# Optimization experiments

Measured on AMD Instinct MI355X. Metric: run time of the kernel, lower is better.

## Reference

```python
import jax, jax.numpy as jnp
import numpy as np

B, LM, LX, D = 16, 1024, 1024, 768


def setup_inputs() -> dict:
    key = jax.random.key(0)
    k1, k2, k3, k4 = jax.random.split(key, 4)
    main = jax.random.normal(k1, (B, LM, D), dtype=jnp.float32)
    x = jax.random.normal(k2, (B, LX, D), dtype=jnp.float32)
    # keras 'uniform' init ~ U(-0.05, 0.05); scale to keep activations sane
    W = jax.random.uniform(k3, (D, D), dtype=jnp.float32, minval=-0.05, maxval=0.05)
    w = jax.random.uniform(k4, (2 * D, 1), dtype=jnp.float32, minval=-0.05, maxval=0.05)
    return {"main": main, "x": x, "W": W, "w": w}


def reference(main, x, W, w):
    # bilinear co-attention scores: (main @ W) . x^T -> (B, LM, LX)
    proj = jnp.einsum('bmd,de->bme', main, W)            # (B, LM, D)
    scores = jnp.einsum('bme,bne->bmn', proj, x)         # (B, LM, LX) -- no softmax in original
    A = jnp.einsum('bmn,bnd->bmd', scores, x)            # attended features (B, LM, D)
    s = main - A
    m = main * A
    outputs = jnp.concatenate([s, m], axis=-1)           # (B, LM, 2D)
    beta = jnp.einsum('bmk,k->bm', outputs, w[:, 0])     # (B, LM) -- raw, no softmax
    pooled = jnp.einsum('bm,bmk->bk', beta, outputs)     # weighted-sum pooling (B, 2D)
    return pooled
```

## Files before the change

### kernel.cpp

```cpp
#include <hip/hip_runtime.h>

constexpr int kB  = 16;
constexpr int kLM = 1024;
constexpr int kLX = 1024;
constexpr int kD  = 768;

using short8 = __attribute__((ext_vector_type(8))) short;
using f32x4  = __attribute__((ext_vector_type(4))) float;

__device__ __forceinline__ unsigned short f2bf(float f) {
    unsigned u = __float_as_uint(f);
    u = (u + 0x7FFF + ((u >> 16) & 1)) >> 16;
    return (unsigned short)u;
}
__device__ __forceinline__ float bf2f(unsigned short h) {
    return __uint_as_float(((unsigned)h) << 16);
}

__device__ __forceinline__ void gl_lds16(const unsigned short* g, unsigned short* l) {
    auto gp = (const __attribute__((address_space(1))) unsigned int*)g;
    auto lp = (__attribute__((address_space(3))) unsigned int*)l;
    __builtin_amdgcn_global_load_lds(gp, lp, 16, 0, 0);
}

__device__ __forceinline__ void writeChunk(unsigned short* dst, float4 lo, float4 hi) {
    union { short8 v; unsigned short u[8]; } o;
    o.u[0] = f2bf(lo.x); o.u[1] = f2bf(lo.y); o.u[2] = f2bf(lo.z); o.u[3] = f2bf(lo.w);
    o.u[4] = f2bf(hi.x); o.u[5] = f2bf(hi.y); o.u[6] = f2bf(hi.z); o.u[7] = f2bf(hi.w);
    *(short8*)dst = o.v;
}

__device__ __forceinline__ size_t chunk_off(int c, int K) {
    int sr = c >> 3, s = c & 7;
    int tt = s ^ (sr & 7);
    int r  = sr * 2 + (tt >> 2);
    int q  = tt & 3;
    return (size_t)r * K + q * 8;
}

__global__ __launch_bounds__(256) void transpose_cvt_kernel(
    const float* __restrict__ x, unsigned short* __restrict__ xT) {
    __shared__ float tile[64][65];
    const int b  = blockIdx.z;
    const int l0 = blockIdx.x * 64;
    const int d0 = blockIdx.y * 64;
    const int t  = threadIdx.x;
    const int tx = t & 15, ty = t >> 4;
    const float* xb = x + ((size_t)b * kLX + l0) * kD + d0;
#pragma unroll
    for (int p = 0; p < 4; ++p) {
        int r = p * 16 + ty;
        float4 v = *(const float4*)(xb + (size_t)r * kD + tx * 4);
        *(float4*)&tile[r][tx * 4] = v;
    }
    __syncthreads();
    unsigned short* xTb = xT + ((size_t)b * kD + d0) * kLX + l0;
#pragma unroll
    for (int p = 0; p < 4; ++p) {
        int dr = p * 16 + ty;
        ushort4 o;
        o.x = f2bf(tile[tx * 4 + 0][dr]);
        o.y = f2bf(tile[tx * 4 + 1][dr]);
        o.z = f2bf(tile[tx * 4 + 2][dr]);
        o.w = f2bf(tile[tx * 4 + 3][dr]);
        *(ushort4*)(xTb + (size_t)dr * kLX + tx * 4) = o;
    }
}

__global__ __launch_bounds__(256) void cvt2_kernel(
    const float* __restrict__ a, unsigned short* __restrict__ oa, int na8,
    const float* __restrict__ b, unsigned short* __restrict__ ob, int nb8) {
    int i = blockIdx.x * 256 + threadIdx.x;
    const float* src;
    unsigned short* dst;
    if (i < na8) {
        src = a + (size_t)i * 8; dst = oa + (size_t)i * 8;
    } else {
        int j = i - na8;
        if (j >= nb8) return;
        src = b + (size_t)j * 8; dst = ob + (size_t)j * 8;
    }
    float4 lo = *(const float4*)src;
    float4 hi = *(const float4*)(src + 4);
    writeChunk(dst, lo, hi);
}

template <bool SYMM>
__global__ __launch_bounds__(256) void gemm_nt_kernel(
    const unsigned short* __restrict__ A, const unsigned short* __restrict__ B,
    unsigned short* __restrict__ C, int M, int N, int K,
    long sA, long sB, long sC, int gx, int gy) {
    __shared__ unsigned short Asm[3][128 * 32];
    __shared__ unsigned short Bsm[3][128 * 32];

    const int wgid = blockIdx.x;
    const int xcd  = wgid & 7;
    const int kk   = wgid >> 3;
    const int tpb  = gx * gy;
    const int grp  = kk / tpb;
    const int til  = kk - grp * tpb;
    const int b    = grp * 8 + xcd;
    const int bi   = til % gx;
    const int bj   = til / gx;
    if (SYMM && bi < bj) return;
    const int i0 = bi * 128, j0 = bj * 128;

    const int t    = threadIdx.x;
    const int wave = t >> 6, lane = t & 63;
    const int wr = (wave >> 1) * 64, wc = (wave & 1) * 64;
    const int quad = lane >> 4, l15 = lane & 15;

    const unsigned short* Ab = A + (size_t)b * sA + (size_t)i0 * K;
    const unsigned short* Bb = B + (size_t)b * sB + (size_t)j0 * K;

    const int c0 = t, c1 = t + 256;
    const size_t off0 = chunk_off(c0, K);
    const size_t off1 = chunk_off(c1, K);

    const int sfr  = ((l15 & 1) * 4 + quad) ^ ((l15 >> 1) & 7);
    const int aOff = wr * 32 + (l15 >> 1) * 64 + sfr * 8;
    const int bOff = wc * 32 + (l15 >> 1) * 64 + sfr * 8;

    f32x4 acc[4][4];
    const f32x4 z = {0.f, 0.f, 0.f, 0.f};
#pragma unroll
    for (int i = 0; i < 4; ++i)
#pragma unroll
        for (int j = 0; j < 4; ++j) acc[i][j] = z;

    const int T = K >> 5;

    gl_lds16(Ab + off0, Asm[0] + c0 * 8);
    gl_lds16(Ab + off1, Asm[0] + c1 * 8);
    gl_lds16(Bb + off0, Bsm[0] + c0 * 8);
    gl_lds16(Bb + off1, Bsm[0] + c1 * 8);
    if (T > 1) {
        gl_lds16(Ab + off0 + 32, Asm[1] + c0 * 8);
        gl_lds16(Ab + off1 + 32, Asm[1] + c1 * 8);
        gl_lds16(Bb + off0 + 32, Bsm[1] + c0 * 8);
        gl_lds16(Bb + off1 + 32, Bsm[1] + c1 * 8);
    }

    int cur = 0;
    for (int kt = 0; kt < T; ++kt) {
        if (kt + 2 < T) {
            int nb = cur + 2; if (nb >= 3) nb -= 3;
            const size_t k = (size_t)(kt + 2) << 5;
            gl_lds16(Ab + off0 + k, Asm[nb] + c0 * 8);
            gl_lds16(Ab + off1 + k, Asm[nb] + c1 * 8);
            gl_lds16(Bb + off0 + k, Bsm[nb] + c0 * 8);
            gl_lds16(Bb + off1 + k, Bsm[nb] + c1 * 8);
            asm volatile("s_waitcnt vmcnt(8)" ::: "memory");
        } else if (kt + 1 < T) {
            asm volatile("s_waitcnt vmcnt(4)" ::: "memory");
        } else {
            asm volatile("s_waitcnt vmcnt(0)" ::: "memory");
        }
        __builtin_amdgcn_s_barrier();
        asm volatile("" ::: "memory");

        const unsigned short* aP = Asm[cur] + aOff;
        const unsigned short* bP = Bsm[cur] + bOff;
        short8 af[4], bg[4];
#pragma unroll
        for (int i = 0; i < 4; ++i) af[i] = *(const short8*)(aP + i * 512);
#pragma unroll
        for (int j = 0; j < 4; ++j) bg[j] = *(const short8*)(bP + j * 512);
        __builtin_amdgcn_s_setprio(1);
#pragma unroll
        for (int i = 0; i < 4; ++i)
#pragma unroll
            for (int j = 0; j < 4; ++j)
                acc[i][j] = __builtin_amdgcn_mfma_f32_16x16x32_bf16(
                    af[i], bg[j], acc[i][j], 0, 0, 0);
        __builtin_amdgcn_s_setprio(0);
        asm volatile("" ::: "memory");
        __builtin_amdgcn_s_barrier();
        cur = cur + 1; if (cur == 3) cur = 0;
    }

    unsigned short* Cb = C + (size_t)b * sC + (size_t)(i0 + wr) * N + j0 + wc;
#pragma unroll
    for (int i = 0; i < 4; ++i)
#pragma unroll
        for (int j = 0; j < 4; ++j)
#pragma unroll
            for (int r = 0; r < 4; ++r)
                Cb[(size_t)(i * 16 + quad * 4 + r) * N + j * 16 + l15] =
                    f2bf(acc[i][j][r]);

    if (SYMM && bi > bj) {
        unsigned short* Cm = C + (size_t)b * sC + (size_t)(j0 + wc) * N + i0 + wr;
#pragma unroll
        for (int i = 0; i < 4; ++i)
#pragma unroll
            for (int j = 0; j < 4; ++j) {
                ushort4 o;
                o.x = f2bf(acc[i][j][0]);
                o.y = f2bf(acc[i][j][1]);
                o.z = f2bf(acc[i][j][2]);
                o.w = f2bf(acc[i][j][3]);
                *(ushort4*)(Cm + (size_t)(j * 16 + l15) * N + i * 16 + quad * 4) = o;
            }
    }
}

__global__ __launch_bounds__(256) void pool_kernel(
    const float* __restrict__ mainp, const unsigned short* __restrict__ Aout,
    const float* __restrict__ w, float* __restrict__ out) {
    __shared__ float red[4][24][64];
    const int b     = blockIdx.y;
    const int chunk = blockIdx.x;
    const int t     = threadIdx.x;
    const int wave  = t >> 6, lane = t & 63;
    float w1[12], w2[12], ps[12], pm[12];
#pragma unroll
    for (int s = 0; s < 12; ++s) {
        w1[s] = w[s * 64 + lane];
        w2[s] = w[kD + s * 64 + lane];
        ps[s] = 0.f; pm[s] = 0.f;
    }
#pragma unroll
    for (int rr = 0; rr < 4; ++rr) {
        const int row = chunk * 16 + rr * 4 + wave;
        const float* mr = mainp + ((size_t)b * kLM + row) * kD;
        const unsigned short* ar = Aout + ((size_t)b * kLM + row) * kD;
        float sv[12], mv[12], acc = 0.f;
#pragma unroll
        for (int s = 0; s < 12; ++s) {
            float m_ = mr[s * 64 + lane];
            float a_ = bf2f(ar[s * 64 + lane]);
            sv[s] = m_ - a_;
            mv[s] = m_ * a_;
            acc += sv[s] * w1[s] + mv[s] * w2[s];
        }
#pragma unroll
        for (int off = 32; off; off >>= 1) acc += __shfl_xor(acc, off);
#pragma unroll
        for (int s = 0; s < 12; ++s) { ps[s] += acc * sv[s]; pm[s] += acc * mv[s]; }
    }
#pragma unroll
    for (int s = 0; s < 12; ++s) {
        red[wave][s][lane]      = ps[s];
        red[wave][12 + s][lane] = pm[s];
    }
    __syncthreads();
    float* ob = out + (size_t)b * 2 * kD;
    for (int v = t; v < 24 * 64; v += 256) {
        const int sl = v >> 6, ln = v & 63;
        const float sum = red[0][sl][ln] + red[1][sl][ln] +
                          red[2][sl][ln] + red[3][sl][ln];
        const int d = (sl < 12) ? sl * 64 + ln : kD + (sl - 12) * 64 + ln;
        atomicAdd(&ob[d], sum);
    }
}

extern "C" void kernel_launch(void* const* d_in, const int* in_sizes, int n_in,
                              void* d_out, int out_size, void* d_ws, size_t ws_size,
                              hipStream_t stream) {
    const float* mainp = (const float*)d_in[0];
    const float* x     = (const float*)d_in[1];
    const float* W     = (const float*)d_in[2];
    const float* w     = (const float*)d_in[3];
    float* out = (float*)d_out;

    char* p = (char*)d_ws;
    unsigned short* xT  = (unsigned short*)p; p += (size_t)kB * kD * kLX * 2;
    unsigned short* G   = (unsigned short*)p; p += (size_t)kB * kD * kD * 2;
    unsigned short* Mt  = (unsigned short*)p; p += (size_t)kB * kD * kD * 2;
    unsigned short* Ao  = (unsigned short*)p; p += (size_t)kB * kLM * kD * 2;
    unsigned short* Wbf = (unsigned short*)p; p += (size_t)kD * kD * 2;
    unsigned short* mainBF = xT;

    hipMemsetAsync(out, 0, (size_t)kB * 2 * kD * sizeof(float), stream);

    transpose_cvt_kernel<<<dim3(kLX / 64, kD / 64, kB), 256, 0, stream>>>(x, xT);

    gemm_nt_kernel<true><<<dim3(kB * 36), 256, 0, stream>>>(
        xT, xT, G, kD, kD, kLX, (long)kD * kLX, (long)kD * kLX, (long)kD * kD,
        6, 6);

    cvt2_kernel<<<dim3((kB * kLM * kD / 8 + kD * kD / 8 + 255) / 256), 256, 0,
                  stream>>>(mainp, mainBF, kB * kLM * kD / 8, W, Wbf,
                            kD * kD / 8);

    gemm_nt_kernel<false><<<dim3(kB * 36), 256, 0, stream>>>(
        G, Wbf, Mt, kD, kD, kD, (long)kD * kD, 0L, (long)kD * kD, 6, 6);

    gemm_nt_kernel<false><<<dim3(kB * 48), 256, 0, stream>>>(
        mainBF, Mt, Ao, kLM, kD, kD, (long)kLM * kD, (long)kD * kD,
        (long)kLM * kD, 8, 6);

    pool_kernel<<<dim3(kLM / 16, kB), 256, 0, stream>>>(mainp, Ao, w, out);
}
```

Before: 230.3 us.

## Reassociate chain as (main·W)·G and merge prep and GEMM launches

The multiplication order changes from main·(W·G) to (main·W)·G. The P=main·W GEMM is independent of the Gram matrix, so it now runs in the same launch as the Gram G=xTᵀx, and the Gram launch uses only lower-triangle tiles via a triangular index. The transpose and convert steps for x, W and main are merged into one prep kernel, and main gets its own bf16 buffer so it no longer aliases xT. The GEMM pipeline drops from three LDS buffers to two, which lowers LDS use but leaves less prefetch slack. The P GEMM over LM=1024 rows costs more FLOPs than the old W·G GEMM over 768 rows, but it removes launches and serial dependencies.

```diff
diff --git a/kernel.cpp b/kernel.cpp
--- a/kernel.cpp
+++ b/kernel.cpp
@@ -38,81 +38,15 @@
     return (size_t)r * K + q * 8;
 }
 
-__global__ __launch_bounds__(256) void transpose_cvt_kernel(
-    const float* __restrict__ x, unsigned short* __restrict__ xT) {
-    __shared__ float tile[64][65];
-    const int b  = blockIdx.z;
-    const int l0 = blockIdx.x * 64;
-    const int d0 = blockIdx.y * 64;
-    const int t  = threadIdx.x;
-    const int tx = t & 15, ty = t >> 4;
-    const float* xb = x + ((size_t)b * kLX + l0) * kD + d0;
-#pragma unroll
-    for (int p = 0; p < 4; ++p) {
-        int r = p * 16 + ty;
-        float4 v = *(const float4*)(xb + (size_t)r * kD + tx * 4);
-        *(float4*)&tile[r][tx * 4] = v;
-    }
-    __syncthreads();
-    unsigned short* xTb = xT + ((size_t)b * kD + d0) * kLX + l0;
-#pragma unroll
-    for (int p = 0; p < 4; ++p) {
-        int dr = p * 16 + ty;
-        ushort4 o;
-        o.x = f2bf(tile[tx * 4 + 0][dr]);
-        o.y = f2bf(tile[tx * 4 + 1][dr]);
-        o.z = f2bf(tile[tx * 4 + 2][dr]);
-        o.w = f2bf(tile[tx * 4 + 3][dr]);
-        *(ushort4*)(xTb + (size_t)dr * kLX + tx * 4) = o;
-    }
-}
-
-__global__ __launch_bounds__(256) void cvt2_kernel(
-    const float* __restrict__ a, unsigned short* __restrict__ oa, int na8,
-    const float* __restrict__ b, unsigned short* __restrict__ ob, int nb8) {
-    int i = blockIdx.x * 256 + threadIdx.x;
-    const float* src;
-    unsigned short* dst;
-    if (i < na8) {
-        src = a + (size_t)i * 8; dst = oa + (size_t)i * 8;
-    } else {
-        int j = i - na8;
-        if (j >= nb8) return;
-        src = b + (size_t)j * 8; dst = ob + (size_t)j * 8;
-    }
-    float4 lo = *(const float4*)src;
-    float4 hi = *(const float4*)(src + 4);
-    writeChunk(dst, lo, hi);
-}
-
-template <bool SYMM>
-__global__ __launch_bounds__(256) void gemm_nt_kernel(
-    const unsigned short* __restrict__ A, const unsigned short* __restrict__ B,
-    unsigned short* __restrict__ C, int M, int N, int K,
-    long sA, long sB, long sC, int gx, int gy) {
-    __shared__ unsigned short Asm[3][128 * 32];
-    __shared__ unsigned short Bsm[3][128 * 32];
-
-    const int wgid = blockIdx.x;
-    const int xcd  = wgid & 7;
-    const int kk   = wgid >> 3;
-    const int tpb  = gx * gy;
-    const int grp  = kk / tpb;
-    const int til  = kk - grp * tpb;
-    const int b    = grp * 8 + xcd;
-    const int bi   = til % gx;
-    const int bj   = til / gx;
-    if (SYMM && bi < bj) return;
-    const int i0 = bi * 128, j0 = bj * 128;
-
+__device__ __forceinline__ void gemm_core(
+    const unsigned short* __restrict__ Ab, const unsigned short* __restrict__ Bb,
+    unsigned short* __restrict__ Cb, unsigned short* __restrict__ Cm,
+    int N, int K, unsigned short* As0, unsigned short* Bs0) {
     const int t    = threadIdx.x;
     const int wave = t >> 6, lane = t & 63;
     const int wr = (wave >> 1) * 64, wc = (wave & 1) * 64;
     const int quad = lane >> 4, l15 = lane & 15;
 
-    const unsigned short* Ab = A + (size_t)b * sA + (size_t)i0 * K;
-    const unsigned short* Bb = B + (size_t)b * sB + (size_t)j0 * K;
-
     const int c0 = t, c1 = t + 256;
     const size_t off0 = chunk_off(c0, K);
     const size_t off1 = chunk_off(c1, K);
@@ -130,37 +64,27 @@
 
     const int T = K >> 5;
 
-    gl_lds16(Ab + off0, Asm[0] + c0 * 8);
-    gl_lds16(Ab + off1, Asm[0] + c1 * 8);
-    gl_lds16(Bb + off0, Bsm[0] + c0 * 8);
-    gl_lds16(Bb + off1, Bsm[0] + c1 * 8);
-    if (T > 1) {
-        gl_lds16(Ab + off0 + 32, Asm[1] + c0 * 8);
-        gl_lds16(Ab + off1 + 32, Asm[1] + c1 * 8);
-        gl_lds16(Bb + off0 + 32, Bsm[1] + c0 * 8);
-        gl_lds16(Bb + off1 + 32, Bsm[1] + c1 * 8);
-    }
-
-    int cur = 0;
+    auto stage = [&](int kt, int sel) {
+        const size_t k = (size_t)kt << 5;
+        unsigned short* Ad = As0 + sel * 4096;
+        unsigned short* Bd = Bs0 + sel * 4096;
+        gl_lds16(Ab + off0 + k, Ad + c0 * 8);
+        gl_lds16(Ab + off1 + k, Ad + c1 * 8);
+        gl_lds16(Bb + off0 + k, Bd + c0 * 8);
+        gl_lds16(Bb + off1 + k, Bd + c1 * 8);
+    };
+
+    stage(0, 0);
+    stage(1, 1);
+
     for (int kt = 0; kt < T; ++kt) {
-        if (kt + 2 < T) {
-            int nb = cur + 2; if (nb >= 3) nb -= 3;
-            const size_t k = (size_t)(kt + 2) << 5;
-            gl_lds16(Ab + off0 + k, Asm[nb] + c0 * 8);
-            gl_lds16(Ab + off1 + k, Asm[nb] + c1 * 8);
-            gl_lds16(Bb + off0 + k, Bsm[nb] + c0 * 8);
-            gl_lds16(Bb + off1 + k, Bsm[nb] + c1 * 8);
-            asm volatile("s_waitcnt vmcnt(8)" ::: "memory");
-        } else if (kt + 1 < T) {
-            asm volatile("s_waitcnt vmcnt(4)" ::: "memory");
-        } else {
-            asm volatile("s_waitcnt vmcnt(0)" ::: "memory");
-        }
+        if (kt + 1 < T) asm volatile("s_waitcnt vmcnt(4)" ::: "memory");
+        else            asm volatile("s_waitcnt vmcnt(0)" ::: "memory");
         __builtin_amdgcn_s_barrier();
         asm volatile("" ::: "memory");
 
-        const unsigned short* aP = Asm[cur] + aOff;
-        const unsigned short* bP = Bsm[cur] + bOff;
+        const unsigned short* aP = As0 + (kt & 1) * 4096 + aOff;
+        const unsigned short* bP = Bs0 + (kt & 1) * 4096 + bOff;
         short8 af[4], bg[4];
 #pragma unroll
         for (int i = 0; i < 4; ++i) af[i] = *(const short8*)(aP + i * 512);
@@ -176,21 +100,21 @@
         __builtin_amdgcn_s_setprio(0);
         asm volatile("" ::: "memory");
         __builtin_amdgcn_s_barrier();
-        cur = cur + 1; if (cur == 3) cur = 0;
-    }
-
-    unsigned short* Cb = C + (size_t)b * sC + (size_t)(i0 + wr) * N + j0 + wc;
+        if (kt + 2 < T) stage(kt + 2, kt & 1);
+    }
+
+    unsigned short* CbW = Cb + (size_t)wr * N + wc;
 #pragma unroll
     for (int i = 0; i < 4; ++i)
 #pragma unroll
         for (int j = 0; j < 4; ++j)
 #pragma unroll
             for (int r = 0; r < 4; ++r)
-                Cb[(size_t)(i * 16 + quad * 4 + r) * N + j * 16 + l15] =
+                CbW[(size_t)(i * 16 + quad * 4 + r) * N + j * 16 + l15] =
                     f2bf(acc[i][j][r]);
 
-    if (SYMM && bi > bj) {
-        unsigned short* Cm = C + (size_t)b * sC + (size_t)(j0 + wc) * N + i0 + wr;
+    if (Cm) {
+        unsigned short* CmW = Cm + (size_t)wc * N + wr;
 #pragma unroll
         for (int i = 0; i < 4; ++i)
 #pragma unroll
@@ -200,9 +124,118 @@
                 o.y = f2bf(acc[i][j][1]);
                 o.z = f2bf(acc[i][j][2]);
                 o.w = f2bf(acc[i][j][3]);
-                *(ushort4*)(Cm + (size_t)(j * 16 + l15) * N + i * 16 + quad * 4) = o;
+                *(ushort4*)(CmW + (size_t)(j * 16 + l15) * N + i * 16 + quad * 4) = o;
             }
     }
+}
+
+__global__ __launch_bounds__(256) void prep_kernel(
+    const float* __restrict__ x, unsigned short* __restrict__ xT,
+    const float* __restrict__ W, unsigned short* __restrict__ WT,
+    const float* __restrict__ mainp, unsigned short* __restrict__ mainBF) {
+    const int bid = blockIdx.x;
+    const int t   = threadIdx.x;
+    if (bid < 3216) {
+        __shared__ float tile[64][65];
+        const float* src;
+        unsigned short* dst;
+        int ss, dstride;
+        if (bid < 3072) {
+            const int lb = bid & 15, rest = bid >> 4;
+            const int db = rest % 12, b = rest / 12;
+            src = x + ((size_t)b * kLX + lb * 64) * kD + db * 64;
+            ss  = kD;
+            dst = xT + ((size_t)b * kD + db * 64) * kLX + lb * 64;
+            dstride = kLX;
+        } else {
+            const int ti = bid - 3072;
+            const int d0 = (ti / 12) * 64, e0 = (ti % 12) * 64;
+            src = W + (size_t)d0 * kD + e0;
+            ss  = kD;
+            dst = WT + (size_t)e0 * kD + d0;
+            dstride = kD;
+        }
+        const int tx = t & 15, ty = t >> 4;
+#pragma unroll
+        for (int p = 0; p < 4; ++p) {
+            int r = p * 16 + ty;
+            float4 v = *(const float4*)(src + (size_t)r * ss + tx * 4);
+            *(float4*)&tile[r][tx * 4] = v;
+        }
+        __syncthreads();
+#pragma unroll
+        for (int p = 0; p < 4; ++p) {
+            int dr = p * 16 + ty;
+            ushort4 o;
+            o.x = f2bf(tile[tx * 4 + 0][dr]);
+            o.y = f2bf(tile[tx * 4 + 1][dr]);
+            o.z = f2bf(tile[tx * 4 + 2][dr]);
+            o.w = f2bf(tile[tx * 4 + 3][dr]);
+            *(ushort4*)(dst + (size_t)dr * dstride + tx * 4) = o;
+        }
+    } else {
+        const long i = (long)(bid - 3216) * 256 + t;
+        const long na8 = (long)kB * kLM * kD / 8;
+        if (i >= na8) return;
+        const float* s = mainp + i * 8;
+        writeChunk(mainBF + i * 8, *(const float4*)s, *(const float4*)(s + 4));
+    }
+}
+
+__global__ __launch_bounds__(256) void gemm_stage2_kernel(
+    const unsigned short* __restrict__ xT,
+    const unsigned short* __restrict__ mainBF,
+    const unsigned short* __restrict__ WT,
+    unsigned short* __restrict__ G, unsigned short* __restrict__ P) {
+    __shared__ unsigned short As[2][4096];
+    __shared__ unsigned short Bs[2][4096];
+    const int wgid = blockIdx.x;
+    const unsigned short *Ab, *Bb;
+    unsigned short *Cb, *Cm = nullptr;
+    int K;
+    if (wgid < 336) {
+        const int xcd = wgid & 7, kk = wgid >> 3;
+        const int grp = kk / 21, til = kk - grp * 21;
+        const int b   = grp * 8 + xcd;
+        int bi = (int)((sqrtf(8.f * (float)til + 1.f) - 1.f) * 0.5f);
+        if (bi * (bi + 1) / 2 > til) --bi;
+        else if ((bi + 1) * (bi + 2) / 2 <= til) ++bi;
+        const int bj = til - bi * (bi + 1) / 2;
+        K = kLX;
+        const unsigned short* base = xT + (size_t)b * kD * kLX;
+        Ab = base + (size_t)bi * 128 * kLX;
+        Bb = base + (size_t)bj * 128 * kLX;
+        unsigned short* Gb = G + (size_t)b * kD * kD;
+        Cb = Gb + (size_t)bi * 128 * kD + bj * 128;
+        if (bi != bj) Cm = Gb + (size_t)bj * 128 * kD + bi * 128;
+    } else {
+        const int pid = wgid - 336;
+        const int xcd = pid & 7, kk = pid >> 3;
+        const int grp = kk / 48, til = kk - grp * 48;
+        const int b   = grp * 8 + xcd;
+        const int bi  = til & 7, bj = til >> 3;
+        K = kD;
+        Ab = mainBF + (size_t)b * kLM * kD + (size_t)bi * 128 * kD;
+        Bb = WT + (size_t)bj * 128 * kD;
+        Cb = P + (size_t)b * kLM * kD + (size_t)bi * 128 * kD + bj * 128;
+    }
+    gemm_core(Ab, Bb, Cb, Cm, kD, K, &As[0][0], &Bs[0][0]);
+}
+
+__global__ __launch_bounds__(256) void gemm_a_kernel(
+    const unsigned short* __restrict__ P, const unsigned short* __restrict__ G,
+    unsigned short* __restrict__ Ao) {
+    __shared__ unsigned short As[2][4096];
+    __shared__ unsigned short Bs[2][4096];
+    const int wgid = blockIdx.x;
+    const int xcd = wgid & 7, kk = wgid >> 3;
+    const int grp = kk / 48, til = kk - grp * 48;
+    const int b   = grp * 8 + xcd;
+    const int bi  = til & 7, bj = til >> 3;
+    const unsigned short* Ab = P + (size_t)b * kLM * kD + (size_t)bi * 128 * kD;
+    const unsigned short* Bb = G + (size_t)b * kD * kD + (size_t)bj * 128 * kD;
+    unsigned short* Cb = Ao + (size_t)b * kLM * kD + (size_t)bi * 128 * kD + bj * 128;
+    gemm_core(Ab, Bb, Cb, nullptr, kD, kD, &As[0][0], &Bs[0][0]);
 }
 
 __global__ __launch_bounds__(256) void pool_kernel(
@@ -265,31 +298,21 @@
     float* out = (float*)d_out;
 
     char* p = (char*)d_ws;
-    unsigned short* xT  = (unsigned short*)p; p += (size_t)kB * kD * kLX * 2;
-    unsigned short* G   = (unsigned short*)p; p += (size_t)kB * kD * kD * 2;
-    unsigned short* Mt  = (unsigned short*)p; p += (size_t)kB * kD * kD * 2;
-    unsigned short* Ao  = (unsigned short*)p; p += (size_t)kB * kLM * kD * 2;
-    unsigned short* Wbf = (unsigned short*)p; p += (size_t)kD * kD * 2;
-    unsigned short* mainBF = xT;
+    unsigned short* xT     = (unsigned short*)p; p += (size_t)kB * kD * kLX * 2;
+    unsigned short* G      = (unsigned short*)p; p += (size_t)kB * kD * kD * 2;
+    unsigned short* P      = (unsigned short*)p; p += (size_t)kB * kLM * kD * 2;
+    unsigned short* Ao     = (unsigned short*)p; p += (size_t)kB * kLM * kD * 2;
+    unsigned short* WT     = (unsigned short*)p; p += (size_t)kD * kD * 2;
+    unsigned short* mainBF = (unsigned short*)p; p += (size_t)kB * kLM * kD * 2;
 
     hipMemsetAsync(out, 0, (size_t)kB * 2 * kD * sizeof(float), stream);
 
-    transpose_cvt_kernel<<<dim3(kLX / 64, kD / 64, kB), 256, 0, stream>>>(x, xT);
-
-    gemm_nt_kernel<true><<<dim3(kB * 36), 256, 0, stream>>>(
-        xT, xT, G, kD, kD, kLX, (long)kD * kLX, (long)kD * kLX, (long)kD * kD,
-        6, 6);
-
-    cvt2_kernel<<<dim3((kB * kLM * kD / 8 + kD * kD / 8 + 255) / 256), 256, 0,
-                  stream>>>(mainp, mainBF, kB * kLM * kD / 8, W, Wbf,
-                            kD * kD / 8);
-
-    gemm_nt_kernel<false><<<dim3(kB * 36), 256, 0, stream>>>(
-        G, Wbf, Mt, kD, kD, kD, (long)kD * kD, 0L, (long)kD * kD, 6, 6);
-
-    gemm_nt_kernel<false><<<dim3(kB * 48), 256, 0, stream>>>(
-        mainBF, Mt, Ao, kLM, kD, kD, (long)kLM * kD, (long)kD * kD,
-        (long)kLM * kD, 8, 6);
+    prep_kernel<<<dim3(3216 + kB * kLM * kD / 8 / 256), 256, 0, stream>>>(
+        x, xT, W, WT, mainp, mainBF);
+
+    gemm_stage2_kernel<<<dim3(336 + 768), 256, 0, stream>>>(xT, mainBF, WT, G, P);
+
+    gemm_a_kernel<<<dim3(768), 256, 0, stream>>>(P, G, Ao);
 
     pool_kernel<<<dim3(kLM / 16, kB), 256, 0, stream>>>(mainp, Ao, w, out);
 }
```

Result: no change. 231.7 us (+0.6%).
